# Kernel optimization log

Measured on AMD Instinct MI355X. Metric: run time of the kernel, lower is better.

## Reference

```python
import jax, jax.numpy as jnp
import numpy as np
import math

D_MODEL = 2048
D_QK = 128
D_V = 128
SEQ = 4096

def setup_inputs() -> dict:
    key = jax.random.key(0)
    ks = jax.random.split(key, 9)
    s = 1.0 / math.sqrt(D_MODEL)
    return {
        "input_q": jax.random.normal(ks[0], (SEQ, D_MODEL), jnp.float32),
        "input_k": jax.random.normal(ks[1], (SEQ, D_MODEL), jnp.float32),
        "input_v": jax.random.normal(ks[2], (SEQ, D_MODEL), jnp.float32),
        "WQ_w": jax.random.normal(ks[3], (D_QK, D_MODEL), jnp.float32) * s,
        "WQ_b": jax.random.normal(ks[4], (D_QK,), jnp.float32) * s,
        "WK_w": jax.random.normal(ks[5], (D_QK, D_MODEL), jnp.float32) * s,
        "WK_b": jax.random.normal(ks[6], (D_QK,), jnp.float32) * s,
        "WV_w": jax.random.normal(ks[7], (D_V, D_MODEL), jnp.float32) * s,
        "WV_b": jax.random.normal(ks[8], (D_V,), jnp.float32) * s,
    }

def reference(input_q, input_k, input_v, WQ_w, WQ_b, WK_w, WK_b, WV_w, WV_b):
    # Linear projections (torch nn.Linear: x @ W.T + b)
    Q = input_q @ WQ_w.T + WQ_b   # [S, d_qk]
    K = input_k @ WK_w.T + WK_b   # [S, d_qk]
    V = input_v @ WV_w.T + WV_b   # [S, d_v]
    S = Q.shape[0]
    # causal mask: -inf strictly above the diagonal, 0 elsewhere
    mask = jnp.triu(jnp.full((S, S), -jnp.inf, dtype=Q.dtype), k=1)
    # NOTE: original code adds mask BEFORE dividing by sqrt(d_model)
    scores = (Q @ K.T + mask) / math.sqrt(D_MODEL)  # [S, S]
    attn = jax.nn.softmax(scores, axis=-1)
    return attn @ V  # [S, d_v]
```

## Files before the change

kernel.cpp:

```cpp
#include <hip/hip_runtime.h>

#define SEQ 4096
#define DM  2048
#define DH  128
#define NSPLIT 8

typedef __attribute__((ext_vector_type(8))) short bf16x8;
typedef __attribute__((ext_vector_type(4))) short short4v;
typedef __attribute__((ext_vector_type(4))) float f32x4;

__device__ inline short f2bf(float f) {
    union { float f; unsigned u; } x; x.f = f;
    unsigned r = x.u + 0x7fffu + ((x.u >> 16) & 1u);
    return (short)(r >> 16);
}

__device__ inline float fexp2(float f) { return __builtin_amdgcn_exp2f(f); }

__global__ __launch_bounds__(256) void convw_kernel(
    const float* __restrict__ wq, const float* __restrict__ wk, const float* __restrict__ wv,
    short* __restrict__ Wbf)
{
    int idx = blockIdx.x * 256 + threadIdx.x;
    int mat = idx >> 16;
    int off = (idx & 65535) * 4;
    const float* W = (mat == 0) ? wq : (mat == 1) ? wk : wv;
    float4 v = *reinterpret_cast<const float4*>(W + off);
    short4v s = { f2bf(v.x), f2bf(v.y), f2bf(v.z), f2bf(v.w) };
    *reinterpret_cast<short4v*>(Wbf + (size_t)mat * DH * DM + off) = s;
}

__global__ __launch_bounds__(256) void proj_kernel(
    const float* __restrict__ inq, const float* __restrict__ ink, const float* __restrict__ inv,
    const short* __restrict__ Wbf,
    const float* __restrict__ bq, const float* __restrict__ bk, const float* __restrict__ bv,
    float* __restrict__ Pqk, float* __restrict__ Pv)
{
    const int mat = blockIdx.y;
    const int s   = blockIdx.z;
    const float* A    = (mat == 0) ? inq : (mat == 1) ? ink : inv;
    const float* bias = (mat == 0) ? bq : (mat == 1) ? bk : bv;

    const int tid  = threadIdx.x;
    const int lane = tid & 63;
    const int w    = tid >> 6;
    const int g    = lane >> 4;
    const int c16  = lane & 15;
    const int i0   = blockIdx.x * 32;
    const int kb   = s * 1024;

    __shared__ short Alds[32][72];
    __shared__ short Wlds[128][72];

    const int ar = tid >> 3, ac = (tid & 7) * 8;
    const float* Aload = A + (size_t)(i0 + ar) * DM + kb + ac;
    const int wr = tid >> 1, wc = (tid & 1) * 32;
    const short* Wload = Wbf + (size_t)mat * DH * DM + (size_t)wr * DM + kb + wc;

    f32x4 acc[4];
    #pragma unroll
    for (int n = 0; n < 4; n++) acc[n] = (f32x4){0.f, 0.f, 0.f, 0.f};

    float4  abuf[4][2];
    bf16x8  wbuf[4][4];

    #pragma unroll
    for (int d = 0; d < 4; d++) {
        #pragma unroll
        for (int j = 0; j < 4; j++)
            wbuf[d][j] = *reinterpret_cast<const bf16x8*>(Wload + d * 64 + j * 8);
        abuf[d][0] = *reinterpret_cast<const float4*>(Aload + d * 64);
        abuf[d][1] = *reinterpret_cast<const float4*>(Aload + d * 64 + 4);
    }

    const int arow = (w >> 1) * 16 + c16;
    const int wbase = (w & 1) * 64;

    #pragma unroll
    for (int c = 0; c < 16; c++) {
        const int d = c & 3;
        {
            short4v s0 = { f2bf(abuf[d][0].x), f2bf(abuf[d][0].y),
                           f2bf(abuf[d][0].z), f2bf(abuf[d][0].w) };
            short4v s1 = { f2bf(abuf[d][1].x), f2bf(abuf[d][1].y),
                           f2bf(abuf[d][1].z), f2bf(abuf[d][1].w) };
            *reinterpret_cast<short4v*>(&Alds[ar][ac])     = s0;
            *reinterpret_cast<short4v*>(&Alds[ar][ac + 4]) = s1;
            #pragma unroll
            for (int j = 0; j < 4; j++)
                *reinterpret_cast<bf16x8*>(&Wlds[wr][wc + j * 8]) = wbuf[d][j];
        }
        if (c + 4 < 16) {
            #pragma unroll
            for (int j = 0; j < 4; j++)
                wbuf[d][j] = *reinterpret_cast<const bf16x8*>(Wload + (c + 4) * 64 + j * 8);
            abuf[d][0] = *reinterpret_cast<const float4*>(Aload + (c + 4) * 64);
            abuf[d][1] = *reinterpret_cast<const float4*>(Aload + (c + 4) * 64 + 4);
        }
        __syncthreads();
        #pragma unroll
        for (int kk = 0; kk < 2; kk++) {
            bf16x8 af = *reinterpret_cast<const bf16x8*>(&Alds[arow][kk * 32 + g * 8]);
            #pragma unroll
            for (int n = 0; n < 4; n++) {
                bf16x8 wf = *reinterpret_cast<const bf16x8*>(
                    &Wlds[wbase + n * 16 + c16][kk * 32 + g * 8]);
                acc[n] = __builtin_amdgcn_mfma_f32_16x16x32_bf16(af, wf, acc[n], 0, 0, 0);
            }
        }
        __syncthreads();
    }

    const int row0 = i0 + (w >> 1) * 16 + g * 4;
    if (mat < 2) {
        float* outp = Pqk + ((size_t)(mat * 2 + s) * SEQ) * DH;
        #pragma unroll
        for (int n = 0; n < 4; n++) {
            int col = wbase + n * 16 + c16;
            float b0 = (s == 0) ? bias[col] : 0.f;
            #pragma unroll
            for (int r = 0; r < 4; r++)
                outp[(size_t)(row0 + r) * DH + col] = acc[n][r] + b0;
        }
    } else {
        float* outp = Pv + (size_t)s * DH * SEQ;
        #pragma unroll
        for (int n = 0; n < 4; n++) {
            int col = wbase + n * 16 + c16;
            float b0 = (s == 0) ? bias[col] : 0.f;
            float4 f = { acc[n][0] + b0, acc[n][1] + b0, acc[n][2] + b0, acc[n][3] + b0 };
            *reinterpret_cast<float4*>(&outp[(size_t)col * SEQ + row0]) = f;
        }
    }
}

__global__ __launch_bounds__(256) void combine_kernel(
    const float* __restrict__ Pqk, const float* __restrict__ Pv,
    short* __restrict__ Qws, short* __restrict__ Kws, short* __restrict__ Vtws)
{
    const int b = blockIdx.x;
    if (b < 1024) {
        int tid = b * 256 + threadIdx.x;
        int mat = tid >> 17;
        int idx4 = (tid & 131071) * 4;
        const float* p0 = Pqk + ((size_t)(mat * 2 + 0) * SEQ) * DH;
        const float* p1 = Pqk + ((size_t)(mat * 2 + 1) * SEQ) * DH;
        float4 a = *reinterpret_cast<const float4*>(p0 + idx4);
        float4 c = *reinterpret_cast<const float4*>(p1 + idx4);
        short4v o = { f2bf(a.x + c.x), f2bf(a.y + c.y), f2bf(a.z + c.z), f2bf(a.w + c.w) };
        short* outp = (mat == 0) ? Qws : Kws;
        *reinterpret_cast<short4v*>(outp + idx4) = o;
    } else {
        int tid = (b - 1024) * 256 + threadIdx.x;
        int idx4 = tid * 4;
        float4 a = *reinterpret_cast<const float4*>(Pv + idx4);
        float4 c = *reinterpret_cast<const float4*>(Pv + (size_t)DH * SEQ + idx4);
        short4v o = { f2bf(a.x + c.x), f2bf(a.y + c.y), f2bf(a.z + c.z), f2bf(a.w + c.w) };
        *reinterpret_cast<short4v*>(Vtws + idx4) = o;
    }
}

__global__ __launch_bounds__(256) void flash_kernel(
    const short* __restrict__ Qws, const short* __restrict__ Kws, const short* __restrict__ Vtws,
    float* __restrict__ Opart, float* __restrict__ mpart, float* __restrict__ lpart)
{
    const int qb = blockIdx.x;
    const int y  = blockIdx.y;
    const int tid = threadIdx.x;
    const int w    = tid >> 6;
    const int lane = tid & 63;
    const int g = lane >> 4, c16 = lane & 15;
    const int i0 = qb * 64 + w * 16;

    __shared__ short Klds[64][136];
    __shared__ short Vlds[128][72];
    __shared__ short Slds[4][16][72];

    const int kkey = tid >> 2,  kdim = (tid & 3) * 32;
    const int vdim = tid >> 1,  vkey = (tid & 1) * 32;

    bf16x8 kreg[4], vreg[4];

    bf16x8 qf[4];
    #pragma unroll
    for (int kk = 0; kk < 4; kk++)
        qf[kk] = *reinterpret_cast<const bf16x8*>(Qws + (size_t)(i0 + c16) * DH + kk * 32 + g * 8);

    float m[4], lsum[4];
    f32x4 O[8];
    #pragma unroll
    for (int r = 0; r < 4; r++) { m[r] = -__builtin_inff(); lsum[r] = 0.f; }
    #pragma unroll
    for (int c = 0; c < 8; c++) O[c] = (f32x4){0.f, 0.f, 0.f, 0.f};

    const float C = 0.03188448666f;

    if (qb >= y) {
        {
            const int j0 = y * 64;
            #pragma unroll
            for (int j = 0; j < 4; j++) {
                kreg[j] = *reinterpret_cast<const bf16x8*>(
                    Kws + (size_t)(j0 + kkey) * DH + kdim + j * 8);
                vreg[j] = *reinterpret_cast<const bf16x8*>(
                    Vtws + (size_t)vdim * SEQ + j0 + vkey + j * 8);
            }
            #pragma unroll
            for (int j = 0; j < 4; j++) {
                *reinterpret_cast<bf16x8*>(&Klds[kkey][kdim + j * 8]) = kreg[j];
                *reinterpret_cast<bf16x8*>(&Vlds[vdim][vkey + j * 8]) = vreg[j];
            }
        }
        __syncthreads();

        for (int jt = y; jt <= qb; jt += NSPLIT) {
            const bool more = (jt + NSPLIT <= qb);
            if (more) {
                const int jn = (jt + NSPLIT) * 64;
                #pragma unroll
                for (int j = 0; j < 4; j++) {
                    kreg[j] = *reinterpret_cast<const bf16x8*>(
                        Kws + (size_t)(jn + kkey) * DH + kdim + j * 8);
                    vreg[j] = *reinterpret_cast<const bf16x8*>(
                        Vtws + (size_t)vdim * SEQ + jn + vkey + j * 8);
                }
            }
            const int j0 = jt * 64;
            f32x4 S[4];
            #pragma unroll
            for (int t = 0; t < 4; t++) S[t] = (f32x4){0.f, 0.f, 0.f, 0.f};
            #pragma unroll
            for (int kk = 0; kk < 4; kk++) {
                #pragma unroll
                for (int t = 0; t < 4; t++) {
                    bf16x8 kf = *reinterpret_cast<const bf16x8*>(
                        &Klds[t * 16 + c16][kk * 32 + g * 8]);
                    S[t] = __builtin_amdgcn_mfma_f32_16x16x32_bf16(qf[kk], kf, S[t], 0, 0, 0);
                }
            }
            float s2[4][4];
            #pragma unroll
            for (int t = 0; t < 4; t++) {
                int key = j0 + t * 16 + c16;
                #pragma unroll
                for (int r = 0; r < 4; r++) {
                    int q = i0 + g * 4 + r;
                    s2[t][r] = (key > q) ? -__builtin_inff() : S[t][r] * C;
                }
            }
            float mnew[4], alpha[4];
            #pragma unroll
            for (int r = 0; r < 4; r++) {
                float rm = fmaxf(fmaxf(s2[0][r], s2[1][r]), fmaxf(s2[2][r], s2[3][r]));
                rm = fmaxf(rm, __shfl_xor(rm, 1));
                rm = fmaxf(rm, __shfl_xor(rm, 2));
                rm = fmaxf(rm, __shfl_xor(rm, 4));
                rm = fmaxf(rm, __shfl_xor(rm, 8));
                mnew[r] = fmaxf(m[r], rm);
                alpha[r] = fexp2(m[r] - mnew[r]);
                m[r] = mnew[r];
            }
            #pragma unroll
            for (int r = 0; r < 4; r++) {
                float ps = 0.f;
                #pragma unroll
                for (int t = 0; t < 4; t++) {
                    float p = fexp2(s2[t][r] - mnew[r]);
                    ps += p;
                    Slds[w][g * 4 + r][t * 16 + c16] = f2bf(p);
                }
                ps += __shfl_xor(ps, 1);
                ps += __shfl_xor(ps, 2);
                ps += __shfl_xor(ps, 4);
                ps += __shfl_xor(ps, 8);
                lsum[r] = lsum[r] * alpha[r] + ps;
                #pragma unroll
                for (int c = 0; c < 8; c++) O[c][r] *= alpha[r];
            }
            #pragma unroll
            for (int kk2 = 0; kk2 < 2; kk2++) {
                bf16x8 pf = *reinterpret_cast<const bf16x8*>(&Slds[w][c16][kk2 * 32 + g * 8]);
                #pragma unroll
                for (int c = 0; c < 8; c++) {
                    bf16x8 vf = *reinterpret_cast<const bf16x8*>(
                        &Vlds[c * 16 + c16][kk2 * 32 + g * 8]);
                    O[c] = __builtin_amdgcn_mfma_f32_16x16x32_bf16(pf, vf, O[c], 0, 0, 0);
                }
            }
            __syncthreads();
            if (more) {
                #pragma unroll
                for (int j = 0; j < 4; j++) {
                    *reinterpret_cast<bf16x8*>(&Klds[kkey][kdim + j * 8]) = kreg[j];
                    *reinterpret_cast<bf16x8*>(&Vlds[vdim][vkey + j * 8]) = vreg[j];
                }
                __syncthreads();
            }
        }
        #pragma unroll
        for (int c = 0; c < 8; c++) {
            int col = c * 16 + c16;
            #pragma unroll
            for (int r = 0; r < 4; r++)
                Opart[((size_t)y * SEQ + i0 + g * 4 + r) * DH + col] = O[c][r];
        }
    }
    if (c16 == 0) {
        #pragma unroll
        for (int r = 0; r < 4; r++) {
            mpart[y * SEQ + i0 + g * 4 + r] = m[r];
            lpart[y * SEQ + i0 + g * 4 + r] = lsum[r];
        }
    }
}

__global__ __launch_bounds__(256) void merge_kernel(
    const float* __restrict__ Opart, const float* __restrict__ mpart, const float* __restrict__ lpart,
    float* __restrict__ out, int NS)
{
    const int row = blockIdx.x * 2 + (threadIdx.x >> 7);
    const int col = threadIdx.x & 127;
    float mh[16];
    float M = -__builtin_inff();
    for (int hh = 0; hh < NS; hh++) {
        mh[hh] = mpart[hh * SEQ + row];
        M = fmaxf(M, mh[hh]);
    }
    float denom = 0.f, num = 0.f;
    for (int hh = 0; hh < NS; hh++) {
        float wgt = fexp2(mh[hh] - M);
        denom += lpart[hh * SEQ + row] * wgt;
        num   += Opart[((size_t)hh * SEQ + row) * DH + col] * wgt;
    }
    out[(size_t)row * DH + col] = num / denom;
}

extern "C" void kernel_launch(void* const* d_in, const int* in_sizes, int n_in,
                              void* d_out, int out_size, void* d_ws, size_t ws_size,
                              hipStream_t stream) {
    const float* inq = (const float*)d_in[0];
    const float* ink = (const float*)d_in[1];
    const float* inv = (const float*)d_in[2];
    const float* wq  = (const float*)d_in[3];
    const float* bq  = (const float*)d_in[4];
    const float* wk  = (const float*)d_in[5];
    const float* bk  = (const float*)d_in[6];
    const float* wv  = (const float*)d_in[7];
    const float* bv  = (const float*)d_in[8];

    char* ws = (char*)d_ws;
    short* Qws   = (short*)(ws);
    short* Kws   = (short*)(ws + (1u << 20));
    short* Vtws  = (short*)(ws + (2u << 20));
    short* Wbf   = (short*)(ws + (3u << 20));
    float* Pqk   = (float*)(ws + 4718592);
    float* Pv    = (float*)(ws + 13107200);
    float* Opart = (float*)(ws + (3u << 20));
    float* mpart = (float*)(ws + (3u << 20) + (size_t)NSPLIT * SEQ * DH * 4);
    float* lpart = mpart + (size_t)NSPLIT * SEQ;

    convw_kernel<<<768, 256, 0, stream>>>(wq, wk, wv, Wbf);
    proj_kernel<<<dim3(128, 3, 2), 256, 0, stream>>>(inq, ink, inv, Wbf, bq, bk, bv, Pqk, Pv);
    combine_kernel<<<1536, 256, 0, stream>>>(Pqk, Pv, Qws, Kws, Vtws);
    flash_kernel<<<dim3(64, NSPLIT), 256, 0, stream>>>(Qws, Kws, Vtws, Opart, mpart, lpart);
    merge_kernel<<<2048, 256, 0, stream>>>(Opart, mpart, lpart, (float*)d_out, NSPLIT);
}
```

Baseline: 188.5 us.

## Enlarge projection row tile to 64 and split K four ways, bias in combine

The projection GEMM now has each block compute 64 rows instead of 32, with every wave doing a 32x64 tile. Each weight tile loaded into LDS is therefore reused across twice as many rows. The reduction dimension is split four ways instead of two, which keeps the grid at 768 blocks. Bias addition moves from the projection epilogue into the combine kernel, and combine now sums four partial buffers instead of two. The cost is double the partial-sum traffic and a larger workspace; the Pv offset is moved to make room.

Result: no change. 184.8 us (-1.9%).

```diff
diff --git a/kernel.cpp b/kernel.cpp
--- a/kernel.cpp
+++ b/kernel.cpp
@@ -33,109 +33,127 @@
 __global__ __launch_bounds__(256) void proj_kernel(
     const float* __restrict__ inq, const float* __restrict__ ink, const float* __restrict__ inv,
     const short* __restrict__ Wbf,
-    const float* __restrict__ bq, const float* __restrict__ bk, const float* __restrict__ bv,
     float* __restrict__ Pqk, float* __restrict__ Pv)
 {
     const int mat = blockIdx.y;
     const int s   = blockIdx.z;
-    const float* A    = (mat == 0) ? inq : (mat == 1) ? ink : inv;
-    const float* bias = (mat == 0) ? bq : (mat == 1) ? bk : bv;
+    const float* A = (mat == 0) ? inq : (mat == 1) ? ink : inv;
 
     const int tid  = threadIdx.x;
     const int lane = tid & 63;
     const int w    = tid >> 6;
     const int g    = lane >> 4;
     const int c16  = lane & 15;
-    const int i0   = blockIdx.x * 32;
-    const int kb   = s * 1024;
-
-    __shared__ short Alds[32][72];
+    const int i0   = blockIdx.x * 64;
+    const int kb   = s * 512;
+
+    __shared__ short Alds[64][72];
     __shared__ short Wlds[128][72];
 
-    const int ar = tid >> 3, ac = (tid & 7) * 8;
+    const int ar = tid >> 2, ac = (tid & 3) * 16;
     const float* Aload = A + (size_t)(i0 + ar) * DM + kb + ac;
     const int wr = tid >> 1, wc = (tid & 1) * 32;
     const short* Wload = Wbf + (size_t)mat * DH * DM + (size_t)wr * DM + kb + wc;
 
-    f32x4 acc[4];
-    #pragma unroll
-    for (int n = 0; n < 4; n++) acc[n] = (f32x4){0.f, 0.f, 0.f, 0.f};
-
-    float4  abuf[4][2];
-    bf16x8  wbuf[4][4];
-
-    #pragma unroll
-    for (int d = 0; d < 4; d++) {
+    f32x4 acc[2][4];
+    #pragma unroll
+    for (int mI = 0; mI < 2; mI++)
+        #pragma unroll
+        for (int n = 0; n < 4; n++) acc[mI][n] = (f32x4){0.f, 0.f, 0.f, 0.f};
+
+    float4  abuf[4][4];
+    bf16x8  wbuf[2][4];
+
+    #pragma unroll
+    for (int d = 0; d < 2; d++) {
         #pragma unroll
         for (int j = 0; j < 4; j++)
             wbuf[d][j] = *reinterpret_cast<const bf16x8*>(Wload + d * 64 + j * 8);
-        abuf[d][0] = *reinterpret_cast<const float4*>(Aload + d * 64);
-        abuf[d][1] = *reinterpret_cast<const float4*>(Aload + d * 64 + 4);
-    }
-
-    const int arow = (w >> 1) * 16 + c16;
-    const int wbase = (w & 1) * 64;
-
-    #pragma unroll
-    for (int c = 0; c < 16; c++) {
-        const int d = c & 3;
+        #pragma unroll
+        for (int j = 0; j < 4; j++)
+            abuf[d][j] = *reinterpret_cast<const float4*>(Aload + d * 64 + j * 4);
+    }
+    #pragma unroll
+    for (int d = 2; d < 4; d++)
+        #pragma unroll
+        for (int j = 0; j < 4; j++)
+            abuf[d][j] = *reinterpret_cast<const float4*>(Aload + d * 64 + j * 4);
+
+    const int rw = (w >> 1) * 32;
+    const int cw = (w & 1) * 64;
+
+    #pragma unroll
+    for (int c = 0; c < 8; c++) {
+        const int da = c & 3, dw = c & 1;
         {
-            short4v s0 = { f2bf(abuf[d][0].x), f2bf(abuf[d][0].y),
-                           f2bf(abuf[d][0].z), f2bf(abuf[d][0].w) };
-            short4v s1 = { f2bf(abuf[d][1].x), f2bf(abuf[d][1].y),
-                           f2bf(abuf[d][1].z), f2bf(abuf[d][1].w) };
-            *reinterpret_cast<short4v*>(&Alds[ar][ac])     = s0;
-            *reinterpret_cast<short4v*>(&Alds[ar][ac + 4]) = s1;
             #pragma unroll
             for (int j = 0; j < 4; j++)
-                *reinterpret_cast<bf16x8*>(&Wlds[wr][wc + j * 8]) = wbuf[d][j];
-        }
-        if (c + 4 < 16) {
+                *reinterpret_cast<bf16x8*>(&Wlds[wr][wc + j * 8]) = wbuf[dw][j];
+            #pragma unroll
+            for (int j = 0; j < 2; j++) {
+                float4 v0 = abuf[da][j * 2], v1 = abuf[da][j * 2 + 1];
+                bf16x8 sv = { f2bf(v0.x), f2bf(v0.y), f2bf(v0.z), f2bf(v0.w),
+                              f2bf(v1.x), f2bf(v1.y), f2bf(v1.z), f2bf(v1.w) };
+                *reinterpret_cast<bf16x8*>(&Alds[ar][ac + j * 8]) = sv;
+            }
+        }
+        if (c + 2 < 8) {
             #pragma unroll
             for (int j = 0; j < 4; j++)
-                wbuf[d][j] = *reinterpret_cast<const bf16x8*>(Wload + (c + 4) * 64 + j * 8);
-            abuf[d][0] = *reinterpret_cast<const float4*>(Aload + (c + 4) * 64);
-            abuf[d][1] = *reinterpret_cast<const float4*>(Aload + (c + 4) * 64 + 4);
+                wbuf[dw][j] = *reinterpret_cast<const bf16x8*>(Wload + (c + 2) * 64 + j * 8);
+        }
+        if (c + 4 < 8) {
+            #pragma unroll
+            for (int j = 0; j < 4; j++)
+                abuf[da][j] = *reinterpret_cast<const float4*>(Aload + (c + 4) * 64 + j * 4);
         }
         __syncthreads();
         #pragma unroll
         for (int kk = 0; kk < 2; kk++) {
-            bf16x8 af = *reinterpret_cast<const bf16x8*>(&Alds[arow][kk * 32 + g * 8]);
+            bf16x8 af0 = *reinterpret_cast<const bf16x8*>(&Alds[rw + c16][kk * 32 + g * 8]);
+            bf16x8 af1 = *reinterpret_cast<const bf16x8*>(&Alds[rw + 16 + c16][kk * 32 + g * 8]);
             #pragma unroll
             for (int n = 0; n < 4; n++) {
                 bf16x8 wf = *reinterpret_cast<const bf16x8*>(
-                    &Wlds[wbase + n * 16 + c16][kk * 32 + g * 8]);
-                acc[n] = __builtin_amdgcn_mfma_f32_16x16x32_bf16(af, wf, acc[n], 0, 0, 0);
+                    &Wlds[cw + n * 16 + c16][kk * 32 + g * 8]);
+                acc[0][n] = __builtin_amdgcn_mfma_f32_16x16x32_bf16(af0, wf, acc[0][n], 0, 0, 0);
+                acc[1][n] = __builtin_amdgcn_mfma_f32_16x16x32_bf16(af1, wf, acc[1][n], 0, 0, 0);
             }
         }
         __syncthreads();
     }
 
-    const int row0 = i0 + (w >> 1) * 16 + g * 4;
     if (mat < 2) {
-        float* outp = Pqk + ((size_t)(mat * 2 + s) * SEQ) * DH;
-        #pragma unroll
-        for (int n = 0; n < 4; n++) {
-            int col = wbase + n * 16 + c16;
-            float b0 = (s == 0) ? bias[col] : 0.f;
-            #pragma unroll
-            for (int r = 0; r < 4; r++)
-                outp[(size_t)(row0 + r) * DH + col] = acc[n][r] + b0;
+        float* outp = Pqk + ((size_t)(mat * 4 + s) * SEQ) * DH;
+        #pragma unroll
+        for (int mI = 0; mI < 2; mI++) {
+            int row0 = i0 + rw + mI * 16 + g * 4;
+            #pragma unroll
+            for (int n = 0; n < 4; n++) {
+                int col = cw + n * 16 + c16;
+                #pragma unroll
+                for (int r = 0; r < 4; r++)
+                    outp[(size_t)(row0 + r) * DH + col] = acc[mI][n][r];
+            }
         }
     } else {
         float* outp = Pv + (size_t)s * DH * SEQ;
         #pragma unroll
-        for (int n = 0; n < 4; n++) {
-            int col = wbase + n * 16 + c16;
-            float b0 = (s == 0) ? bias[col] : 0.f;
-            float4 f = { acc[n][0] + b0, acc[n][1] + b0, acc[n][2] + b0, acc[n][3] + b0 };
-            *reinterpret_cast<float4*>(&outp[(size_t)col * SEQ + row0]) = f;
+        for (int mI = 0; mI < 2; mI++) {
+            int row0 = i0 + rw + mI * 16 + g * 4;
+            #pragma unroll
+            for (int n = 0; n < 4; n++) {
+                int col = cw + n * 16 + c16;
+                float4 f = { acc[mI][n][0], acc[mI][n][1], acc[mI][n][2], acc[mI][n][3] };
+                *reinterpret_cast<float4*>(&outp[(size_t)col * SEQ + row0]) = f;
+            }
         }
     }
 }
 
 __global__ __launch_bounds__(256) void combine_kernel(
     const float* __restrict__ Pqk, const float* __restrict__ Pv,
+    const float* __restrict__ bq, const float* __restrict__ bk, const float* __restrict__ bv,
     short* __restrict__ Qws, short* __restrict__ Kws, short* __restrict__ Vtws)
 {
     const int b = blockIdx.x;
@@ -143,19 +161,31 @@
         int tid = b * 256 + threadIdx.x;
         int mat = tid >> 17;
         int idx4 = (tid & 131071) * 4;
-        const float* p0 = Pqk + ((size_t)(mat * 2 + 0) * SEQ) * DH;
-        const float* p1 = Pqk + ((size_t)(mat * 2 + 1) * SEQ) * DH;
-        float4 a = *reinterpret_cast<const float4*>(p0 + idx4);
-        float4 c = *reinterpret_cast<const float4*>(p1 + idx4);
-        short4v o = { f2bf(a.x + c.x), f2bf(a.y + c.y), f2bf(a.z + c.z), f2bf(a.w + c.w) };
+        float4 acc = {0.f, 0.f, 0.f, 0.f};
+        #pragma unroll
+        for (int s = 0; s < 4; s++) {
+            float4 p = *reinterpret_cast<const float4*>(
+                Pqk + ((size_t)(mat * 4 + s) * SEQ) * DH + idx4);
+            acc.x += p.x; acc.y += p.y; acc.z += p.z; acc.w += p.w;
+        }
+        const float* bias = (mat == 0) ? bq : bk;
+        int col = idx4 & (DH - 1);
+        acc.x += bias[col]; acc.y += bias[col + 1]; acc.z += bias[col + 2]; acc.w += bias[col + 3];
+        short4v o = { f2bf(acc.x), f2bf(acc.y), f2bf(acc.z), f2bf(acc.w) };
         short* outp = (mat == 0) ? Qws : Kws;
         *reinterpret_cast<short4v*>(outp + idx4) = o;
     } else {
         int tid = (b - 1024) * 256 + threadIdx.x;
         int idx4 = tid * 4;
-        float4 a = *reinterpret_cast<const float4*>(Pv + idx4);
-        float4 c = *reinterpret_cast<const float4*>(Pv + (size_t)DH * SEQ + idx4);
-        short4v o = { f2bf(a.x + c.x), f2bf(a.y + c.y), f2bf(a.z + c.z), f2bf(a.w + c.w) };
+        float4 acc = {0.f, 0.f, 0.f, 0.f};
+        #pragma unroll
+        for (int s = 0; s < 4; s++) {
+            float4 p = *reinterpret_cast<const float4*>(Pv + (size_t)s * DH * SEQ + idx4);
+            acc.x += p.x; acc.y += p.y; acc.z += p.z; acc.w += p.w;
+        }
+        float bvv = bv[idx4 >> 12];
+        acc.x += bvv; acc.y += bvv; acc.z += bvv; acc.w += bvv;
+        short4v o = { f2bf(acc.x), f2bf(acc.y), f2bf(acc.z), f2bf(acc.w) };
         *reinterpret_cast<short4v*>(Vtws + idx4) = o;
     }
 }
@@ -354,14 +384,14 @@
     short* Vtws  = (short*)(ws + (2u << 20));
     short* Wbf   = (short*)(ws + (3u << 20));
     float* Pqk   = (float*)(ws + 4718592);
-    float* Pv    = (float*)(ws + 13107200);
+    float* Pv    = (float*)(ws + 21495808);
     float* Opart = (float*)(ws + (3u << 20));
     float* mpart = (float*)(ws + (3u << 20) + (size_t)NSPLIT * SEQ * DH * 4);
     float* lpart = mpart + (size_t)NSPLIT * SEQ;
 
     convw_kernel<<<768, 256, 0, stream>>>(wq, wk, wv, Wbf);
-    proj_kernel<<<dim3(128, 3, 2), 256, 0, stream>>>(inq, ink, inv, Wbf, bq, bk, bv, Pqk, Pv);
-    combine_kernel<<<1536, 256, 0, stream>>>(Pqk, Pv, Qws, Kws, Vtws);
+    proj_kernel<<<dim3(64, 3, 4), 256, 0, stream>>>(inq, ink, inv, Wbf, Pqk, Pv);
+    combine_kernel<<<1536, 256, 0, stream>>>(Pqk, Pv, bq, bk, bv, Qws, Kws, Vtws);
     flash_kernel<<<dim3(64, NSPLIT), 256, 0, stream>>>(Qws, Kws, Vtws, Opart, mpart, lpart);
     merge_kernel<<<2048, 256, 0, stream>>>(Opart, mpart, lpart, (float*)d_out, NSPLIT);
 }
```
